# Optimization experiments

Hardware: AMD Instinct MI355X
Metric: run time of the kernel (lower is better)

Reference implementation:

```python
import jax, jax.numpy as jnp
import numpy as np

N_EMBD = 512
N_HEAD = 8
HEAD = N_EMBD // N_HEAD
EPS = 1e-5

def layernorm(x, g, b):
    mu = jnp.mean(x, axis=-1, keepdims=True)
    var = jnp.mean(jnp.square(x - mu), axis=-1, keepdims=True)
    return (x - mu) * jax.lax.rsqrt(var + EPS) * g + b

def setup_inputs() -> dict:
    key = jax.random.key(0)
    ks = jax.random.split(key, 12)
    B, T, C, H, D = 32, 512, N_EMBD, N_HEAD, HEAD
    s = lambda fan: 1.0 / np.sqrt(fan)
    return {
        "x": jax.random.normal(ks[0], (B, T, C), jnp.float32),
        "wq": jax.random.normal(ks[1], (H, C, D), jnp.float32) * s(C),
        "wk": jax.random.normal(ks[2], (H, C, D), jnp.float32) * s(C),
        "wv": jax.random.normal(ks[3], (H, C, D), jnp.float32) * s(C),
        "w_proj": jax.random.normal(ks[4], (C, C), jnp.float32) * s(C),
        "b_proj": jnp.zeros((C,), jnp.float32),
        "w1": jax.random.normal(ks[5], (C, 4 * C), jnp.float32) * s(C),
        "b1": jnp.zeros((4 * C,), jnp.float32),
        "w2": jax.random.normal(ks[6], (4 * C, C), jnp.float32) * s(4 * C),
        "b2": jnp.zeros((C,), jnp.float32),
        "ln1_g": jnp.ones((C,), jnp.float32),
        "ln1_b": jnp.zeros((C,), jnp.float32),
        "ln2_g": jnp.ones((C,), jnp.float32),
        "ln2_b": jnp.zeros((C,), jnp.float32),
    }

def reference(x, wq, wk, wv, w_proj, b_proj, w1, b1, w2, b2, ln1_g, ln1_b, ln2_g, ln2_b):
    B, T, C = x.shape
    h = layernorm(x, ln1_g, ln1_b)
    q = jnp.einsum('btc,hcd->bhtd', h, wq)
    k = jnp.einsum('btc,hcd->bhtd', h, wk)
    v = jnp.einsum('btc,hcd->bhtd', h, wv)
    # NB: original scales by n_embd**-0.5 (C), not head_size
    scores = jnp.einsum('bhtd,bhsd->bhts', q, k) * (C ** -0.5)
    causal = jnp.tril(jnp.ones((T, T), bool))
    scores = jnp.where(causal, scores, -jnp.inf)
    attn = jax.nn.softmax(scores, axis=-1)
    o = jnp.einsum('bhts,bhsd->bhtd', attn, v)  # [B,H,T,D]
    o = jnp.transpose(o, (0, 2, 1, 3)).reshape(B, T, C)  # concat heads
    x = x + o @ w_proj + b_proj
    h2 = layernorm(x, ln2_g, ln2_b)
    ffn = jax.nn.relu(h2 @ w1 + b1) @ w2 + b2
    return x + ffn
```

## Files before the change

### kernel.cpp

```cpp
#include <hip/hip_runtime.h>
#include <hip/hip_bf16.h>


#define B_  32
#define T_  512
#define C_  512
#define H_  8
#define D_  64
#define BT  (B_*T_)
#define CF  2048

typedef __hip_bfloat16 bf16;
typedef __attribute__((ext_vector_type(8))) short bf16x8;
typedef __attribute__((ext_vector_type(4))) float f32x4;
typedef __attribute__((ext_vector_type(4))) short short4v;

__device__ __forceinline__ float bf2f(bf16 x) { return __bfloat162float(x); }
__device__ __forceinline__ bf16  f2bf(float x){ return __float2bfloat16(x); }
__device__ __forceinline__ short f2bf_bits(float f){
    bf16 h = __float2bfloat16(f);
    return *reinterpret_cast<short*>(&h);
}
__device__ __forceinline__ float bfbits2f(short s){
    unsigned u = ((unsigned)(unsigned short)s) << 16;
    return __uint_as_float(u);
}

#define AS_G __attribute__((address_space(1)))
#define AS_L __attribute__((address_space(3)))

#define SCHED_FENCE() __builtin_amdgcn_sched_barrier(0)

__global__ __launch_bounds__(256) void transpose_all(const float* __restrict__ wq,
                                                     const float* __restrict__ wk,
                                                     const float* __restrict__ wv,
                                                     const float* __restrict__ wproj,
                                                     const float* __restrict__ w1,
                                                     const float* __restrict__ w2,
                                                     bf16* __restrict__ wt)
{
    const int t = blockIdx.x;
    const float* src; int K, Nn, k0, n0; size_t dstoff;
    if (t < 192) {
        const int which = t / 64, w = t % 64, hh = w >> 3, kt = w & 7;
        src = (which == 0 ? wq : which == 1 ? wk : wv) + (size_t)hh * 512 * 64;
        K = 512; Nn = 64; k0 = kt * 64; n0 = 0;
        dstoff = (size_t)(which * 512 + hh * 64) * 512;
    } else if (t < 256) {
        const int i = t - 192;
        src = wproj; K = 512; Nn = 512; n0 = (i & 7) * 64; k0 = (i >> 3) * 64;
        dstoff = (size_t)1536 * 512;
    } else if (t < 512) {
        const int i = t - 256;
        src = w1; K = 512; Nn = 2048; n0 = (i & 31) * 64; k0 = (i >> 5) * 64;
        dstoff = (size_t)2048 * 512;
    } else {
        const int i = t - 512;
        src = w2; K = 2048; Nn = 512; n0 = (i & 7) * 64; k0 = (i >> 3) * 64;
        dstoff = (size_t)2048 * 512 + (size_t)2048 * 512;
    }

    __shared__ float tl[64][65];
    const int tid = threadIdx.x;
    #pragma unroll
    for (int j = 0; j < 16; ++j) {
        const int e = j * 256 + tid, r = e >> 6, c = e & 63;
        tl[r][c] = src[(size_t)(k0 + r) * Nn + n0 + c];
    }
    __syncthreads();
    #pragma unroll
    for (int j = 0; j < 16; ++j) {
        const int e = j * 256 + tid, n = e >> 6, kk = e & 63;
        wt[dstoff + (size_t)(n0 + n) * K + k0 + kk] = f2bf(tl[kk][n]);
    }
}

__global__ __launch_bounds__(256) void ln_kernel(const float* __restrict__ x,
                                                 const float* __restrict__ g,
                                                 const float* __restrict__ b,
                                                 bf16* __restrict__ out)
{
    const int row = blockIdx.x;
    const int tid = threadIdx.x;
    const float* xr = x + (size_t)row * C_;
    float v0 = xr[tid], v1 = xr[tid + 256];

    __shared__ float red[4];

    float s = v0 + v1;
    #pragma unroll
    for (int off = 32; off > 0; off >>= 1) s += __shfl_down(s, off, 64);
    if ((tid & 63) == 0) red[tid >> 6] = s;
    __syncthreads();
    const float mean = (red[0] + red[1] + red[2] + red[3]) * (1.0f / C_);
    __syncthreads();

    float d0 = v0 - mean, d1 = v1 - mean;
    float vs = d0 * d0 + d1 * d1;
    #pragma unroll
    for (int off = 32; off > 0; off >>= 1) vs += __shfl_down(vs, off, 64);
    if ((tid & 63) == 0) red[tid >> 6] = vs;
    __syncthreads();
    const float var  = (red[0] + red[1] + red[2] + red[3]) * (1.0f / C_);
    const float rstd = rsqrtf(var + 1e-5f);

    bf16* orow = out + (size_t)row * C_;
    orow[tid]       = f2bf(d0 * rstd * g[tid]       + b[tid]);
    orow[tid + 256] = f2bf(d1 * rstd * g[tid + 256] + b[tid + 256]);
}

template<bool QKV, bool RELU, bool OUT_BF16>
__global__ __launch_bounds__(256, 2) void mfma_gemm(const bf16* __restrict__ A,
                                                    const bf16* __restrict__ Bt,
                                                    const float* __restrict__ bias,
                                                    const float* __restrict__ res,
                                                    void* __restrict__ outp,
                                                    int N, int K)
{
    __shared__ __align__(16) bf16 As[2][128 * 64];
    __shared__ __align__(16) bf16 Bs[2][128 * 64];

    const int tid  = threadIdx.x;
    const int wave = tid >> 6, lane = tid & 63;
    const int l16  = lane & 15, quad = lane >> 4;
    const int wm   = wave >> 1, wn = wave & 1;

    const int nwg = gridDim.x * gridDim.y;
    int bid = blockIdx.y * gridDim.x + blockIdx.x;
    bid = (bid & 7) * (nwg >> 3) + (bid >> 3);
    const int tn = (bid % gridDim.x) * 128;
    const int tm = (bid / gridDim.x) * 128;
    const bool vblk = QKV && (tn >= 1024);

    f32x4 acc[4][4];
    #pragma unroll
    for (int i = 0; i < 4; ++i)
        #pragma unroll
        for (int j = 0; j < 4; ++j) acc[i][j] = (f32x4){0.f, 0.f, 0.f, 0.f};

    auto STAGE = [&](int buf, int k0) {
        #pragma unroll
        for (int j = 0; j < 4; ++j) {
            const int g = j * 256 + tid;
            const int row = g >> 3, phys = g & 7;
            const int c = phys ^ (row & 7);
            __builtin_amdgcn_global_load_lds((const AS_G void*)(A  + (size_t)(tm + row) * K + k0 + c * 8),
                                             (AS_L void*)&As[buf][(size_t)g * 8], 16, 0, 0);
            __builtin_amdgcn_global_load_lds((const AS_G void*)(Bt + (size_t)(tn + row) * K + k0 + c * 8),
                                             (AS_L void*)&Bs[buf][(size_t)g * 8], 16, 0, 0);
        }
    };

    STAGE(0, 0);
    __syncthreads();

    int cur = 0;
    for (int k0 = 0; k0 < K; k0 += 64) {
        if (k0 + 64 < K) STAGE(cur ^ 1, k0 + 64);

        #pragma unroll
        for (int half = 0; half < 2; ++half) {
            bf16x8 af[4], bfr[4];
            #pragma unroll
            for (int mf = 0; mf < 4; ++mf) {
                const int r = wm * 64 + mf * 16 + l16;
                const int p = (half * 4 + quad) ^ (r & 7);
                af[mf] = *(const bf16x8*)&As[cur][r * 64 + p * 8];
            }
            #pragma unroll
            for (int nf = 0; nf < 4; ++nf) {
                const int r = wn * 64 + nf * 16 + l16;
                const int p = (half * 4 + quad) ^ (r & 7);
                bfr[nf] = *(const bf16x8*)&Bs[cur][r * 64 + p * 8];
            }
            if (vblk) {
                #pragma unroll
                for (int mf = 0; mf < 4; ++mf)
                    #pragma unroll
                    for (int nf = 0; nf < 4; ++nf)
                        acc[mf][nf] = __builtin_amdgcn_mfma_f32_16x16x32_bf16(af[mf], bfr[nf], acc[mf][nf], 0, 0, 0);
            } else {
                #pragma unroll
                for (int mf = 0; mf < 4; ++mf)
                    #pragma unroll
                    for (int nf = 0; nf < 4; ++nf)
                        acc[mf][nf] = __builtin_amdgcn_mfma_f32_16x16x32_bf16(bfr[nf], af[mf], acc[mf][nf], 0, 0, 0);
            }
        }

        __syncthreads();
        cur ^= 1;
    }

    {
        #pragma unroll
        for (int mf = 0; mf < 4; ++mf) {
            const int m = tm + wm * 64 + mf * 16 + l16;
            #pragma unroll
            for (int nf = 0; nf < 4; ++nf) {
                const int nb = tn + wn * 64 + nf * 16 + quad * 4;
                f32x4 a = acc[mf][nf];
                if (bias) a += *(const f32x4*)&bias[nb];
                if (RELU) {
                    #pragma unroll
                    for (int r = 0; r < 4; ++r) a[r] = fmaxf(a[r], 0.0f);
                }
                if (res)  a += *(const f32x4*)&res[(size_t)m * N + nb];
                if (OUT_BF16) {
                    short4v pk;
                    #pragma unroll
                    for (int r = 0; r < 4; ++r) pk[r] = f2bf_bits(a[r]);
                    *(short4v*)&((bf16*)outp)[(size_t)m * N + nb] = pk;
                } else {
                    *(f32x4*)&((float*)outp)[(size_t)m * N + nb] = a;
                }
            }
        }
    }
}

template<bool QKV, bool RELU, bool OUT_BF16>
__global__ __launch_bounds__(512, 2) void gemm8ph(const bf16* __restrict__ A,
                                                  const bf16* __restrict__ Bt,
                                                  const float* __restrict__ bias,
                                                  const float* __restrict__ res,
                                                  void* __restrict__ outp,
                                                  int N, int K)
{
    extern __shared__ __align__(16) char smem[];
    bf16* const As0 = (bf16*)smem;
    bf16* const As1 = As0 + 256 * 64;
    bf16* const Bs0 = As1 + 256 * 64;
    bf16* const Bs1 = Bs0 + 256 * 64;

    const int tid  = threadIdx.x;
    const int lane = tid & 63, wid = tid >> 6;
    const int l16  = lane & 15, quad = lane >> 4;
    const int wm   = wid >> 2, wn = wid & 3;

    const int gridx = gridDim.x;
    const int nwg   = gridx * gridDim.y;
    int bid = blockIdx.y * gridx + blockIdx.x;
    bid = (bid & 7) * (nwg >> 3) + (bid >> 3);
    const int tn = (bid % gridx) * 256;
    const int tm = (bid / gridx) * 256;
    const bool vblk = QKV && (tn >= 1024);
    const int NT = K >> 6, NI = NT >> 1;

    f32x4 acc[2][4][4];
    #pragma unroll
    for (int q = 0; q < 2; ++q)
        #pragma unroll
        for (int i = 0; i < 4; ++i)
            #pragma unroll
            for (int j = 0; j < 4; ++j) acc[q][i][j] = (f32x4){0.f, 0.f, 0.f, 0.f};

    bf16x8 af[4][2], bfr[4][2];

#define SA8(dst, u, h) do {                                                          \
    const int _k0 = (u) << 6;                                                        \
    _Pragma("unroll")                                                                \
    for (int _j = 0; _j < 2; ++_j) {                                                 \
        const int _g = (h) * 1024 + _j * 512 + tid;                                  \
        const int _r = _g >> 3, _p = _g & 7;                                         \
        const int _c = _p ^ (_r & 7);                                                \
        __builtin_amdgcn_global_load_lds((const AS_G void*)(A + (size_t)(tm + _r) * K + _k0 + _c * 8), \
                                         (AS_L void*)((dst) + _g * 8), 16, 0, 0);    \
    } } while (0)

#define SB8(dst, u, h) do {                                                          \
    const int _k0 = (u) << 6;                                                        \
    _Pragma("unroll")                                                                \
    for (int _j = 0; _j < 2; ++_j) {                                                 \
        const int _g = (h) * 1024 + _j * 512 + tid;                                  \
        const int _r = _g >> 3, _p = _g & 7;                                         \
        const int _c = _p ^ (_r & 7);                                                \
        __builtin_amdgcn_global_load_lds((const AS_G void*)(Bt + (size_t)(tn + _r) * K + _k0 + _c * 8), \
                                         (AS_L void*)((dst) + _g * 8), 16, 0, 0);    \
    } } while (0)

#define LDA8(Ab, qm) do {                                                            \
    _Pragma("unroll")                                                                \
    for (int _mf = 0; _mf < 4; ++_mf)                                                \
        _Pragma("unroll")                                                            \
        for (int _kh = 0; _kh < 2; ++_kh) {                                          \
            const int _r = wm * 128 + (qm) * 64 + _mf * 16 + l16;                    \
            const int _p = (_kh * 4 + quad) ^ (_r & 7);                              \
            af[_mf][_kh] = *(const bf16x8*)&(Ab)[_r * 64 + _p * 8];                  \
        } } while (0)

#define LDB8(Bb, qn) do {                                                            \
    _Pragma("unroll")                                                                \
    for (int _c2 = 0; _c2 < 2; ++_c2)                                                \
        _Pragma("unroll")                                                            \
        for (int _kh = 0; _kh < 2; ++_kh) {                                          \
            const int _nf = (qn) * 2 + _c2;                                          \
            const int _r = wn * 64 + _nf * 16 + l16;                                 \
            const int _p = (_kh * 4 + quad) ^ (_r & 7);                              \
            bfr[_nf][_kh] = *(const bf16x8*)&(Bb)[_r * 64 + _p * 8];                 \
        } } while (0)

#define MM8(qm, qn) do {                                                             \
    __builtin_amdgcn_s_setprio(1);                                                   \
    _Pragma("unroll")                                                                \
    for (int _mf = 0; _mf < 4; ++_mf)                                                \
        _Pragma("unroll")                                                            \
        for (int _c2 = 0; _c2 < 2; ++_c2) {                                          \
            const int _nf = (qn) * 2 + _c2;                                          \
            _Pragma("unroll")                                                        \
            for (int _kh = 0; _kh < 2; ++_kh) {                                      \
                if (vblk) acc[qm][_mf][_nf] = __builtin_amdgcn_mfma_f32_16x16x32_bf16(af[_mf][_kh], bfr[_nf][_kh], acc[qm][_mf][_nf], 0, 0, 0); \
                else      acc[qm][_mf][_nf] = __builtin_amdgcn_mfma_f32_16x16x32_bf16(bfr[_nf][_kh], af[_mf][_kh], acc[qm][_mf][_nf], 0, 0, 0); \
            }                                                                        \
        }                                                                            \
    __builtin_amdgcn_s_setprio(0);                                                   \
    } while (0)

#define GATE8() do { SCHED_FENCE(); __builtin_amdgcn_s_barrier();                    \
    asm volatile("s_waitcnt lgkmcnt(0)" ::: "memory"); SCHED_FENCE(); } while (0)
#define ENDP8() do { SCHED_FENCE(); __builtin_amdgcn_s_barrier(); SCHED_FENCE(); } while (0)

    SA8(As0, 0, 0); SA8(As0, 0, 1);
    SB8(Bs0, 0, 0); SB8(Bs0, 0, 1);
    SB8(Bs1, 1, 0); SB8(Bs1, 1, 1);
    asm volatile("s_waitcnt vmcnt(4)" ::: "memory");
    SCHED_FENCE();
    __builtin_amdgcn_s_barrier();
    SCHED_FENCE();

    for (int i = 0; i < NI; ++i) {
        const int t1 = 2 * i + 1, t2 = 2 * i + 2, t3 = 2 * i + 3;
        const bool p2 = t2 < NT, p3 = t3 < NT, lastI = (i == NI - 1);

        LDA8(As0, 0); LDB8(Bs0, 0);
        SA8(As1, t1, 0);
        GATE8(); MM8(0, 0); ENDP8();
        LDB8(Bs0, 1);
        SA8(As1, t1, 1);
        GATE8(); MM8(0, 1); ENDP8();
        LDA8(As0, 1);
        if (p2) SB8(Bs0, t2, 0);
        GATE8(); MM8(1, 1); ENDP8();
        if (p2) SA8(As0, t2, 0);
        if (lastI) asm volatile("s_waitcnt vmcnt(0)" ::: "memory");
        else       asm volatile("s_waitcnt vmcnt(4)" ::: "memory");
        GATE8(); MM8(1, 0); ENDP8();
        LDA8(As1, 0); LDB8(Bs1, 0);
        if (p2) SA8(As0, t2, 1);
        GATE8(); MM8(0, 0); ENDP8();
        LDB8(Bs1, 1);
        if (p2) SB8(Bs0, t2, 1);
        GATE8(); MM8(0, 1); ENDP8();
        LDA8(As1, 1);
        if (p3) SB8(Bs1, t3, 0);
        GATE8(); MM8(1, 1); ENDP8();
        if (p3) SB8(Bs1, t3, 1);
        if (lastI) asm volatile("s_waitcnt vmcnt(0)" ::: "memory");
        else       asm volatile("s_waitcnt vmcnt(4)" ::: "memory");
        GATE8(); MM8(1, 0); ENDP8();
    }

#undef SA8
#undef SB8
#undef LDA8
#undef LDB8
#undef MM8
#undef GATE8
#undef ENDP8

    if (QKV) {
        bf16* qkv = (bf16*)outp;
        if (!vblk) {
            const int which = tn >> 9;
            bf16* dst = qkv + (size_t)which * (8u << 20);
            #pragma unroll
            for (int qm = 0; qm < 2; ++qm)
                #pragma unroll
                for (int mf = 0; mf < 4; ++mf) {
                    const int m = tm + wm * 128 + qm * 64 + mf * 16 + l16;
                    const int bb = m >> 9, t = m & 511;
                    #pragma unroll
                    for (int nf = 0; nf < 4; ++nf) {
                        const int nb = tn + wn * 64 + nf * 16 + quad * 4;
                        const int hh = (nb >> 6) & 7, dd = nb & 63;
                        short4v pk;
                        #pragma unroll
                        for (int r = 0; r < 4; ++r) pk[r] = f2bf_bits(acc[qm][mf][nf][r]);
                        *(short4v*)&dst[((size_t)(bb * 8 + hh) * 512 + t) * 64 + dd] = pk;
                    }
                }
        } else {
            bf16* dst = qkv + (size_t)2 * (8u << 20);
            #pragma unroll
            for (int qm = 0; qm < 2; ++qm)
                #pragma unroll
                for (int mf = 0; mf < 4; ++mf) {
                    const int mb = tm + wm * 128 + qm * 64 + mf * 16 + quad * 4;
                    const int bb = mb >> 9, t = mb & 511;
                    #pragma unroll
                    for (int nf = 0; nf < 4; ++nf) {
                        const int n = tn + wn * 64 + nf * 16 + l16;
                        const int hh = (n >> 6) & 7, dd = n & 63;
                        short4v pk;
                        #pragma unroll
                        for (int r = 0; r < 4; ++r) pk[r] = f2bf_bits(acc[qm][mf][nf][r]);
                        *(short4v*)&dst[((size_t)(bb * 8 + hh) * 64 + dd) * 512 + t] = pk;
                    }
                }
        }
    } else {
        #pragma unroll
        for (int qm = 0; qm < 2; ++qm)
            #pragma unroll
            for (int mf = 0; mf < 4; ++mf) {
                const int m = tm + wm * 128 + qm * 64 + mf * 16 + l16;
                #pragma unroll
                for (int nf = 0; nf < 4; ++nf) {
                    const int nb = tn + wn * 64 + nf * 16 + quad * 4;
                    f32x4 a = acc[qm][mf][nf];
                    if (bias) a += *(const f32x4*)&bias[nb];
                    if (RELU) {
                        #pragma unroll
                        for (int r = 0; r < 4; ++r) a[r] = fmaxf(a[r], 0.0f);
                    }
                    if (res)  a += *(const f32x4*)&res[(size_t)m * N + nb];
                    if (OUT_BF16) {
                        short4v pk;
                        #pragma unroll
                        for (int r = 0; r < 4; ++r) pk[r] = f2bf_bits(a[r]);
                        *(short4v*)&((bf16*)outp)[(size_t)m * N + nb] = pk;
                    } else {
                        *(f32x4*)&((float*)outp)[(size_t)m * N + nb] = a;
                    }
                }
            }
    }
}

#define ATTN_TILE(qa, m_i, l_i, Of, qw, qtT)                                          \
  do {                                                                                \
    f32x4 Sf[4];                                                                      \
    _Pragma("unroll")                                                                 \
    for (int kf = 0; kf < 4; ++kf) {                                                  \
        const int row = kf * 16 + l16;                                                \
        bf16x8 b0 = *(const bf16x8*)&Ks[cur][row * 64 + ((quad ^ (row & 7)) * 8)];    \
        bf16x8 b1 = *(const bf16x8*)&Ks[cur][row * 64 + (((4 + quad) ^ (row & 7)) * 8)]; \
        f32x4 z = (f32x4){0.f, 0.f, 0.f, 0.f};                                        \
        z = __builtin_amdgcn_mfma_f32_16x16x32_bf16(qa[0], b0, z, 0, 0, 0);           \
        z = __builtin_amdgcn_mfma_f32_16x16x32_bf16(qa[1], b1, z, 0, 0, 0);           \
        Sf[kf] = z;                                                                   \
    }                                                                                 \
    if (kt == qtT) {                                                                  \
        _Pragma("unroll")                                                             \
        for (int kf = 0; kf < 4; ++kf)                                                \
            _Pragma("unroll")                                                         \
            for (int r = 0; r < 4; ++r)                                               \
                if (kt * 64 + kf * 16 + l16 > (qw) + quad * 4 + r) Sf[kf][r] = -1e30f;\
    }                                                                                 \
    float mnew[4], alpha[4];                                                          \
    _Pragma("unroll")                                                                 \
    for (int r = 0; r < 4; ++r) {                                                     \
        float v = fmaxf(fmaxf(Sf[0][r], Sf[1][r]), fmaxf(Sf[2][r], Sf[3][r]));        \
        v = fmaxf(v, __shfl_xor(v, 1, 64));                                           \
        v = fmaxf(v, __shfl_xor(v, 2, 64));                                           \
        v = fmaxf(v, __shfl_xor(v, 4, 64));                                           \
        v = fmaxf(v, __shfl_xor(v, 8, 64));                                           \
        mnew[r]   = fmaxf(m_i[r], v);                                                 \
        alpha[r]  = __expf(m_i[r] - mnew[r]);                                         \
        m_i[r]    = mnew[r];                                                          \
    }                                                                                 \
    float rs[4] = {0.f, 0.f, 0.f, 0.f};                                               \
    _Pragma("unroll")                                                                 \
    for (int kf = 0; kf < 4; ++kf) {                                                  \
        _Pragma("unroll")                                                             \
        for (int r = 0; r < 4; ++r) {                                                 \
            float p = __expf(Sf[kf][r] - mnew[r]);                                    \
            rs[r] += p;                                                               \
            Pw[wave][quad * 4 + r][kf * 16 + l16] = f2bf(p);                          \
        }                                                                             \
    }                                                                                 \
    _Pragma("unroll")                                                                 \
    for (int r = 0; r < 4; ++r) {                                                     \
        rs[r] += __shfl_xor(rs[r], 1, 64);                                            \
        rs[r] += __shfl_xor(rs[r], 2, 64);                                            \
        rs[r] += __shfl_xor(rs[r], 4, 64);                                            \
        rs[r] += __shfl_xor(rs[r], 8, 64);                                            \
        l_i[r] = l_i[r] * alpha[r] + rs[r];                                           \
    }                                                                                 \
    _Pragma("unroll")                                                                 \
    for (int f = 0; f < 4; ++f)                                                       \
        _Pragma("unroll")                                                             \
        for (int r = 0; r < 4; ++r)                                                   \
            Of[f][r] *= alpha[r];                                                     \
    bf16x8 pa0 = *(const bf16x8*)&Pw[wave][l16][quad * 8];                            \
    bf16x8 pa1 = *(const bf16x8*)&Pw[wave][l16][32 + quad * 8];                       \
    _Pragma("unroll")                                                                 \
    for (int f = 0; f < 4; ++f) {                                                     \
        const int vrow = f * 16 + l16;                                                \
        bf16x8 vb0 = *(const bf16x8*)&Vt[cur][vrow * 64 + ((quad ^ (vrow & 7)) * 8)]; \
        bf16x8 vb1 = *(const bf16x8*)&Vt[cur][vrow * 64 + (((4 + quad) ^ (vrow & 7)) * 8)]; \
        Of[f] = __builtin_amdgcn_mfma_f32_16x16x32_bf16(pa0, vb0, Of[f], 0, 0, 0);    \
        Of[f] = __builtin_amdgcn_mfma_f32_16x16x32_bf16(pa1, vb1, Of[f], 0, 0, 0);    \
    }                                                                                 \
  } while (0)

__global__ __launch_bounds__(256, 2) void attn_kernel(const bf16* __restrict__ q,
                                                      const bf16* __restrict__ kM,
                                                      const bf16* __restrict__ vT,
                                                      bf16* __restrict__ o)
{
    __shared__ __align__(16) bf16 Ks[2][64 * 64];
    __shared__ __align__(16) bf16 Vt[2][64 * 64];
    __shared__ __align__(16) bf16 Pw[4][16][72];

    const int tid  = threadIdx.x;
    const int wave = tid >> 6, lane = tid & 63;
    const int l16  = lane & 15, quad = lane >> 4;

    const int nwg = gridDim.x * gridDim.y;
    int bid = blockIdx.y * gridDim.x + blockIdx.x;
    bid = (bid & 7) * (nwg >> 3) + (bid >> 3);
    const int pair = bid & 3;
    const int bh   = bid >> 2;

    const int qt0 = pair, qt1 = 7 - pair;
    const int qw0 = qt0 * 64 + wave * 16;
    const int qw1 = qt1 * 64 + wave * 16;

    const float scale = 0.04419417382415922f;
    bf16x8 qa0[2], qa1[2];
    #pragma unroll
    for (int c = 0; c < 2; ++c) {
        bf16x8 t0 = *(const bf16x8*)(q + ((size_t)bh * T_ + qw0 + l16) * 64 + c * 32 + quad * 8);
        bf16x8 t1 = *(const bf16x8*)(q + ((size_t)bh * T_ + qw1 + l16) * 64 + c * 32 + quad * 8);
        #pragma unroll
        for (int j = 0; j < 8; ++j) {
            t0[j] = f2bf_bits(bfbits2f(t0[j]) * scale);
            t1[j] = f2bf_bits(bfbits2f(t1[j]) * scale);
        }
        qa0[c] = t0; qa1[c] = t1;
    }

    float m0[4], l0[4], m1[4], l1[4];
    f32x4 O0[4], O1[4];
    #pragma unroll
    for (int r = 0; r < 4; ++r) { m0[r] = -1e30f; l0[r] = 0.f; m1[r] = -1e30f; l1[r] = 0.f; }
    #pragma unroll
    for (int f = 0; f < 4; ++f) { O0[f] = (f32x4){0.f,0.f,0.f,0.f}; O1[f] = (f32x4){0.f,0.f,0.f,0.f}; }

    auto STAGE = [&](int buf, int kt) {
        const int k0 = kt * 64;
        #pragma unroll
        for (int j = 0; j < 2; ++j) {
            const int g = j * 256 + tid;
            const int row = g >> 3, phys = g & 7;
            const int c = phys ^ (row & 7);
            __builtin_amdgcn_global_load_lds((const AS_G void*)(kM + ((size_t)bh * T_ + k0 + row) * 64 + c * 8),
                                             (AS_L void*)&Ks[buf][(size_t)g * 8], 16, 0, 0);
            __builtin_amdgcn_global_load_lds((const AS_G void*)(vT + ((size_t)bh * 64 + row) * T_ + k0 + c * 8),
                                             (AS_L void*)&Vt[buf][(size_t)g * 8], 16, 0, 0);
        }
    };

    STAGE(0, 0);
    __syncthreads();

    int cur = 0;
    for (int kt = 0; kt <= qt1; ++kt) {
        if (kt < qt1) STAGE(cur ^ 1, kt + 1);

        if (kt <= qt0) ATTN_TILE(qa0, m0, l0, O0, qw0, qt0);
        ATTN_TILE(qa1, m1, l1, O1, qw1, qt1);

        __syncthreads();
        cur ^= 1;
    }

    const int b = bh >> 3, hh = bh & 7;
    #pragma unroll
    for (int r = 0; r < 4; ++r) {
        const float inv0 = 1.0f / l0[r];
        const float inv1 = 1.0f / l1[r];
        const int t0 = qw0 + quad * 4 + r;
        const int t1 = qw1 + quad * 4 + r;
        #pragma unroll
        for (int f = 0; f < 4; ++f) {
            o[((size_t)b * T_ + t0) * C_ + hh * 64 + f * 16 + l16] = f2bf(O0[f][r] * inv0);
            o[((size_t)b * T_ + t1) * C_ + hh * 64 + f * 16 + l16] = f2bf(O1[f][r] * inv1);
        }
    }
}

extern "C" void kernel_launch(void* const* d_in, const int* in_sizes, int n_in,
                              void* d_out, int out_size, void* d_ws, size_t ws_size,
                              hipStream_t stream)
{
    const float* x     = (const float*)d_in[0];
    const float* wq    = (const float*)d_in[1];
    const float* wk    = (const float*)d_in[2];
    const float* wv    = (const float*)d_in[3];
    const float* wproj = (const float*)d_in[4];
    const float* bproj = (const float*)d_in[5];
    const float* w1    = (const float*)d_in[6];
    const float* b1    = (const float*)d_in[7];
    const float* w2    = (const float*)d_in[8];
    const float* b2    = (const float*)d_in[9];
    const float* ln1g  = (const float*)d_in[10];
    const float* ln1b  = (const float*)d_in[11];
    const float* ln2g  = (const float*)d_in[12];
    const float* ln2b  = (const float*)d_in[13];

    char* ws = (char*)d_ws;
    bf16*  h    = (bf16*)(ws + 0);
    bf16*  q    = (bf16*)(ws + ((size_t)16 << 20));
    bf16*  k    = (bf16*)(ws + ((size_t)32 << 20));
    bf16*  v    = (bf16*)(ws + ((size_t)48 << 20));
    bf16*  mid  = (bf16*)(ws + 0);
    bf16*  o    = (bf16*)(ws + ((size_t)64 << 20));
    bf16*  h2   = (bf16*)(ws + ((size_t)80 << 20));
    bf16*  wt   = (bf16*)(ws + ((size_t)96 << 20));
    bf16*  projt = wt + (size_t)1536 * 512;
    bf16*  w1t   = wt + (size_t)2048 * 512;
    bf16*  w2t   = wt + (size_t)4096 * 512;
    float* x1    = (float*)d_out;

    static bool smem_init = false;
    if (!smem_init) {
        smem_init = true;
        hipFuncSetAttribute(reinterpret_cast<const void*>(&gemm8ph<true,  false, true>),
                            hipFuncAttributeMaxDynamicSharedMemorySize, 131072);
        hipFuncSetAttribute(reinterpret_cast<const void*>(&gemm8ph<false, true,  true>),
                            hipFuncAttributeMaxDynamicSharedMemorySize, 131072);
    }

    transpose_all<<<768, 256, 0, stream>>>(wq, wk, wv, wproj, w1, w2, wt);

    ln_kernel<<<BT, 256, 0, stream>>>(x, ln1g, ln1b, h);

    gemm8ph<true,  false, true><<<dim3(6, 64), 512, 131072, stream>>>(h, wt, nullptr, nullptr, q, 1536, 512);

    attn_kernel<<<dim3(4, B_ * H_), 256, 0, stream>>>(q, k, v, o);

    mfma_gemm<false, false, false><<<dim3(4, 128), 256, 0, stream>>>(o, projt, bproj, x, x1, 512, 512);

    ln_kernel<<<BT, 256, 0, stream>>>(x1, ln2g, ln2b, h2);

    gemm8ph<false, true,  true><<<dim3(8, 64), 512, 131072, stream>>>(h2, w1t, b1, nullptr, mid, 2048, 512);

    mfma_gemm<false, false, false><<<dim3(4, 128), 256, 0, stream>>>(mid, w2t, b2, x1, (float*)d_out, 512, 2048);
}
```

Measured before the change: 349.2 us.

## Add 256x128 two-phase pipelined GEMM for QKV and FFN2 projections

Introduces gemm4ph, a 512-thread kernel with a 256x128 tile, double-buffered global-to-LDS loads and a two-phase barrier-gated MFMA schedule using setprio, sized for two workgroups per CU. The QKV projection moves from the 256x256 gemm8ph to this kernel with twice as many blocks, and the FFN down-projection (K=2048) moves off the simpler mfma_gemm onto it. The 256x256 gemm8ph loses its QKV layout branch and keeps only the FFN-up path. The aim is better occupancy and grid fill for the smaller-N GEMMs; the cost is lower per-block operand reuse and more complex scheduling.

```diff
diff --git a/kernel.cpp b/kernel.cpp
--- a/kernel.cpp
+++ b/kernel.cpp
@@ -130,7 +130,6 @@
     bid = (bid & 7) * (nwg >> 3) + (bid >> 3);
     const int tn = (bid % gridDim.x) * 128;
     const int tm = (bid / gridDim.x) * 128;
-    const bool vblk = QKV && (tn >= 1024);
 
     f32x4 acc[4][4];
     #pragma unroll
@@ -173,19 +172,11 @@
                 const int p = (half * 4 + quad) ^ (r & 7);
                 bfr[nf] = *(const bf16x8*)&Bs[cur][r * 64 + p * 8];
             }
-            if (vblk) {
+            #pragma unroll
+            for (int mf = 0; mf < 4; ++mf)
                 #pragma unroll
-                for (int mf = 0; mf < 4; ++mf)
-                    #pragma unroll
-                    for (int nf = 0; nf < 4; ++nf)
-                        acc[mf][nf] = __builtin_amdgcn_mfma_f32_16x16x32_bf16(af[mf], bfr[nf], acc[mf][nf], 0, 0, 0);
-            } else {
-                #pragma unroll
-                for (int mf = 0; mf < 4; ++mf)
-                    #pragma unroll
-                    for (int nf = 0; nf < 4; ++nf)
-                        acc[mf][nf] = __builtin_amdgcn_mfma_f32_16x16x32_bf16(bfr[nf], af[mf], acc[mf][nf], 0, 0, 0);
-            }
+                for (int nf = 0; nf < 4; ++nf)
+                    acc[mf][nf] = __builtin_amdgcn_mfma_f32_16x16x32_bf16(bfr[nf], af[mf], acc[mf][nf], 0, 0, 0);
         }
 
         __syncthreads();
@@ -335,25 +326,32 @@
         LDA8(As0, 0); LDB8(Bs0, 0);
         SA8(As1, t1, 0);
         GATE8(); MM8(0, 0); ENDP8();
+
         LDB8(Bs0, 1);
         SA8(As1, t1, 1);
         GATE8(); MM8(0, 1); ENDP8();
+
         LDA8(As0, 1);
         if (p2) SB8(Bs0, t2, 0);
         GATE8(); MM8(1, 1); ENDP8();
+
         if (p2) SA8(As0, t2, 0);
         if (lastI) asm volatile("s_waitcnt vmcnt(0)" ::: "memory");
         else       asm volatile("s_waitcnt vmcnt(4)" ::: "memory");
         GATE8(); MM8(1, 0); ENDP8();
+
         LDA8(As1, 0); LDB8(Bs1, 0);
         if (p2) SA8(As0, t2, 1);
         GATE8(); MM8(0, 0); ENDP8();
+
         LDB8(Bs1, 1);
         if (p2) SB8(Bs0, t2, 1);
         GATE8(); MM8(0, 1); ENDP8();
+
         LDA8(As1, 1);
         if (p3) SB8(Bs1, t3, 0);
         GATE8(); MM8(1, 1); ENDP8();
+
         if (p3) SB8(Bs1, t3, 1);
         if (lastI) asm volatile("s_waitcnt vmcnt(0)" ::: "memory");
         else       asm volatile("s_waitcnt vmcnt(4)" ::: "memory");
@@ -368,6 +366,164 @@
 #undef GATE8
 #undef ENDP8
 
+    {
+        #pragma unroll
+        for (int qm = 0; qm < 2; ++qm)
+            #pragma unroll
+            for (int mf = 0; mf < 4; ++mf) {
+                const int m = tm + wm * 128 + qm * 64 + mf * 16 + l16;
+                #pragma unroll
+                for (int nf = 0; nf < 4; ++nf) {
+                    const int nb = tn + wn * 64 + nf * 16 + quad * 4;
+                    f32x4 a = acc[qm][mf][nf];
+                    if (bias) a += *(const f32x4*)&bias[nb];
+                    if (RELU) {
+                        #pragma unroll
+                        for (int r = 0; r < 4; ++r) a[r] = fmaxf(a[r], 0.0f);
+                    }
+                    if (res)  a += *(const f32x4*)&res[(size_t)m * N + nb];
+                    if (OUT_BF16) {
+                        short4v pk;
+                        #pragma unroll
+                        for (int r = 0; r < 4; ++r) pk[r] = f2bf_bits(a[r]);
+                        *(short4v*)&((bf16*)outp)[(size_t)m * N + nb] = pk;
+                    } else {
+                        *(f32x4*)&((float*)outp)[(size_t)m * N + nb] = a;
+                    }
+                }
+            }
+    }
+}
+
+template<bool QKV, bool RELU, bool OUT_BF16>
+__global__ __launch_bounds__(512, 2) void gemm4ph(const bf16* __restrict__ A,
+                                                  const bf16* __restrict__ Bt,
+                                                  const float* __restrict__ bias,
+                                                  const float* __restrict__ res,
+                                                  void* __restrict__ outp,
+                                                  int N, int K)
+{
+    extern __shared__ __align__(16) char smem[];
+    bf16* const Asl = (bf16*)smem;
+    bf16* const Bsl = Asl + 2 * 256 * 64;
+
+    const int tid  = threadIdx.x;
+    const int lane = tid & 63, wid = tid >> 6;
+    const int l16  = lane & 15, quad = lane >> 4;
+    const int wm   = wid >> 2, wn = wid & 3;
+
+    const int gridx = gridDim.x;
+    const int nwg   = gridx * gridDim.y;
+    int bid = blockIdx.y * gridx + blockIdx.x;
+    bid = (bid & 7) * (nwg >> 3) + (bid >> 3);
+    const int tn = (bid % gridx) * 128;
+    const int tm = (bid / gridx) * 256;
+    const bool vblk = QKV && (tn >= 1024);
+    const int NT = K >> 6;
+
+    f32x4 acc[2][4][2];
+    #pragma unroll
+    for (int q = 0; q < 2; ++q)
+        #pragma unroll
+        for (int i = 0; i < 4; ++i)
+            #pragma unroll
+            for (int j = 0; j < 2; ++j) acc[q][i][j] = (f32x4){0.f, 0.f, 0.f, 0.f};
+
+    bf16x8 af[4][2], bfr[2][2];
+
+#define SAQ4(u, q) do {                                                              \
+    bf16* _dst = Asl + ((u) & 1) * (256 * 64);                                       \
+    const int _k0 = (u) << 6;                                                        \
+    _Pragma("unroll")                                                                \
+    for (int _jj = 0; _jj < 2; ++_jj) {                                              \
+        const int _g = ((q) + _jj * 2) * 512 + tid;                                  \
+        const int _r = _g >> 3, _p = _g & 7;                                         \
+        const int _c = _p ^ (_r & 7);                                                \
+        __builtin_amdgcn_global_load_lds((const AS_G void*)(A + (size_t)(tm + _r) * K + _k0 + _c * 8), \
+                                         (AS_L void*)(_dst + _g * 8), 16, 0, 0);     \
+    } } while (0)
+
+#define SB4(u) do {                                                                  \
+    bf16* _dst = Bsl + ((u) & 1) * (128 * 64);                                       \
+    const int _k0 = (u) << 6;                                                        \
+    _Pragma("unroll")                                                                \
+    for (int _jj = 0; _jj < 2; ++_jj) {                                              \
+        const int _g = _jj * 512 + tid;                                              \
+        const int _r = _g >> 3, _p = _g & 7;                                         \
+        const int _c = _p ^ (_r & 7);                                                \
+        __builtin_amdgcn_global_load_lds((const AS_G void*)(Bt + (size_t)(tn + _r) * K + _k0 + _c * 8), \
+                                         (AS_L void*)(_dst + _g * 8), 16, 0, 0);     \
+    } } while (0)
+
+#define LDA4(Ab, qm) do {                                                            \
+    _Pragma("unroll")                                                                \
+    for (int _mf = 0; _mf < 4; ++_mf)                                                \
+        _Pragma("unroll")                                                            \
+        for (int _kh = 0; _kh < 2; ++_kh) {                                          \
+            const int _r = wm * 128 + (qm) * 64 + _mf * 16 + l16;                    \
+            const int _p = (_kh * 4 + quad) ^ (_r & 7);                              \
+            af[_mf][_kh] = *(const bf16x8*)&(Ab)[_r * 64 + _p * 8];                  \
+        } } while (0)
+
+#define LDB4(Bb) do {                                                                \
+    _Pragma("unroll")                                                                \
+    for (int _nf = 0; _nf < 2; ++_nf)                                                \
+        _Pragma("unroll")                                                            \
+        for (int _kh = 0; _kh < 2; ++_kh) {                                          \
+            const int _r = wn * 32 + _nf * 16 + l16;                                 \
+            const int _p = (_kh * 4 + quad) ^ (_r & 7);                              \
+            bfr[_nf][_kh] = *(const bf16x8*)&(Bb)[_r * 64 + _p * 8];                 \
+        } } while (0)
+
+#define MM4(qm) do {                                                                 \
+    __builtin_amdgcn_s_setprio(1);                                                   \
+    _Pragma("unroll")                                                                \
+    for (int _mf = 0; _mf < 4; ++_mf)                                                \
+        _Pragma("unroll")                                                            \
+        for (int _nf = 0; _nf < 2; ++_nf)                                            \
+            _Pragma("unroll")                                                        \
+            for (int _kh = 0; _kh < 2; ++_kh) {                                      \
+                if (vblk) acc[qm][_mf][_nf] = __builtin_amdgcn_mfma_f32_16x16x32_bf16(af[_mf][_kh], bfr[_nf][_kh], acc[qm][_mf][_nf], 0, 0, 0); \
+                else      acc[qm][_mf][_nf] = __builtin_amdgcn_mfma_f32_16x16x32_bf16(bfr[_nf][_kh], af[_mf][_kh], acc[qm][_mf][_nf], 0, 0, 0); \
+            }                                                                        \
+    __builtin_amdgcn_s_setprio(0);                                                   \
+    } while (0)
+
+#define GATE4() do { SCHED_FENCE(); __builtin_amdgcn_s_barrier();                    \
+    asm volatile("s_waitcnt lgkmcnt(0)" ::: "memory"); SCHED_FENCE(); } while (0)
+#define ENDP4() do { SCHED_FENCE(); __builtin_amdgcn_s_barrier(); SCHED_FENCE(); } while (0)
+
+    SB4(0); SAQ4(0, 0); SAQ4(0, 1);
+    if (NT > 1) { SB4(1); SAQ4(1, 0); }
+    if (NT > 1) asm volatile("s_waitcnt vmcnt(4)" ::: "memory");
+    else        asm volatile("s_waitcnt vmcnt(0)" ::: "memory");
+    SCHED_FENCE();
+    __builtin_amdgcn_s_barrier();
+    SCHED_FENCE();
+
+    for (int t = 0; t < NT; ++t) {
+        bf16* const Ab = Asl + (t & 1) * (256 * 64);
+        bf16* const Bb = Bsl + (t & 1) * (128 * 64);
+
+        LDB4(Bb); LDA4(Ab, 0);
+        if (t + 1 < NT) SAQ4(t + 1, 1);
+        GATE4(); MM4(0); ENDP4();
+
+        LDA4(Ab, 1);
+        if (t + 2 < NT) { SB4(t + 2); SAQ4(t + 2, 0); }
+        if (t + 2 < NT) asm volatile("s_waitcnt vmcnt(4)" ::: "memory");
+        else            asm volatile("s_waitcnt vmcnt(0)" ::: "memory");
+        GATE4(); MM4(1); ENDP4();
+    }
+
+#undef SAQ4
+#undef SB4
+#undef LDA4
+#undef LDB4
+#undef MM4
+#undef GATE4
+#undef ENDP4
+
     if (QKV) {
         bf16* qkv = (bf16*)outp;
         if (!vblk) {
@@ -380,8 +536,8 @@
                     const int m = tm + wm * 128 + qm * 64 + mf * 16 + l16;
                     const int bb = m >> 9, t = m & 511;
                     #pragma unroll
-                    for (int nf = 0; nf < 4; ++nf) {
-                        const int nb = tn + wn * 64 + nf * 16 + quad * 4;
+                    for (int nf = 0; nf < 2; ++nf) {
+                        const int nb = tn + wn * 32 + nf * 16 + quad * 4;
                         const int hh = (nb >> 6) & 7, dd = nb & 63;
                         short4v pk;
                         #pragma unroll
@@ -398,8 +554,8 @@
                     const int mb = tm + wm * 128 + qm * 64 + mf * 16 + quad * 4;
                     const int bb = mb >> 9, t = mb & 511;
                     #pragma unroll
-                    for (int nf = 0; nf < 4; ++nf) {
-                        const int n = tn + wn * 64 + nf * 16 + l16;
+                    for (int nf = 0; nf < 2; ++nf) {
+                        const int n = tn + wn * 32 + nf * 16 + l16;
                         const int hh = (n >> 6) & 7, dd = n & 63;
                         short4v pk;
                         #pragma unroll
@@ -415,8 +571,8 @@
             for (int mf = 0; mf < 4; ++mf) {
                 const int m = tm + wm * 128 + qm * 64 + mf * 16 + l16;
                 #pragma unroll
-                for (int nf = 0; nf < 4; ++nf) {
-                    const int nb = tn + wn * 64 + nf * 16 + quad * 4;
+                for (int nf = 0; nf < 2; ++nf) {
+                    const int nb = tn + wn * 32 + nf * 16 + quad * 4;
                     f32x4 a = acc[qm][mf][nf];
                     if (bias) a += *(const f32x4*)&bias[nb];
                     if (RELU) {
@@ -627,17 +783,19 @@
     static bool smem_init = false;
     if (!smem_init) {
         smem_init = true;
-        hipFuncSetAttribute(reinterpret_cast<const void*>(&gemm8ph<true,  false, true>),
-                            hipFuncAttributeMaxDynamicSharedMemorySize, 131072);
-        hipFuncSetAttribute(reinterpret_cast<const void*>(&gemm8ph<false, true,  true>),
-                            hipFuncAttributeMaxDynamicSharedMemorySize, 131072);
+        (void)hipFuncSetAttribute(reinterpret_cast<const void*>(&gemm8ph<false, true,  true>),
+                                  hipFuncAttributeMaxDynamicSharedMemorySize, 131072);
+        (void)hipFuncSetAttribute(reinterpret_cast<const void*>(&gemm4ph<true,  false, true>),
+                                  hipFuncAttributeMaxDynamicSharedMemorySize, 98304);
+        (void)hipFuncSetAttribute(reinterpret_cast<const void*>(&gemm4ph<false, false, false>),
+                                  hipFuncAttributeMaxDynamicSharedMemorySize, 98304);
     }
 
     transpose_all<<<768, 256, 0, stream>>>(wq, wk, wv, wproj, w1, w2, wt);
 
     ln_kernel<<<BT, 256, 0, stream>>>(x, ln1g, ln1b, h);
 
-    gemm8ph<true,  false, true><<<dim3(6, 64), 512, 131072, stream>>>(h, wt, nullptr, nullptr, q, 1536, 512);
+    gemm4ph<true,  false, true><<<dim3(12, 64), 512, 98304, stream>>>(h, wt, nullptr, nullptr, q, 1536, 512);
 
     attn_kernel<<<dim3(4, B_ * H_), 256, 0, stream>>>(q, k, v, o);
 
@@ -647,5 +805,5 @@
 
     gemm8ph<false, true,  true><<<dim3(8, 64), 512, 131072, stream>>>(h2, w1t, b1, nullptr, mid, 2048, 512);
 
-    mfma_gemm<false, false, false><<<dim3(4, 128), 256, 0, stream>>>(mid, w2t, b2, x1, (float*)d_out, 512, 2048);
+    gemm4ph<false, false, false><<<dim3(4, 64), 512, 98304, stream>>>(mid, w2t, b2, x1, (float*)d_out, 512, 2048);
 }
```

After: 343.9 us. Within noise of the previous version (-1.5%).
